# Performance work log

Hardware: AMD Instinct MI355X
Metric: run time of the kernel (lower is better)

## Reference

```python
import jax, jax.numpy as jnp
import numpy as np

B, L, E, H, D = 32, 512, 256, 8, 64
SCALE = int(D ** 0.5)  # matches TF: int(hidden_dim ** 0.5) == 8


def setup_inputs() -> dict:
    key = jax.random.key(0)
    ks = jax.random.split(key, 6)
    return {
        "x": jax.random.normal(ks[0], (B, L, E), dtype=jnp.float32),
        "positional": jax.random.normal(ks[1], (L, E), dtype=jnp.float32) * 0.02,
        "Wq": jax.random.normal(ks[2], (H, E, D), dtype=jnp.float32) * 0.05,
        "Wk": jax.random.normal(ks[3], (H, E, D), dtype=jnp.float32) * 0.05,
        "Wv": jax.random.normal(ks[4], (H, E, D), dtype=jnp.float32) * 0.05,
        "Wo": jax.random.normal(ks[5], (H * D, E), dtype=jnp.float32) * 0.05,
    }


def reference(x, positional, Wq, Wk, Wv, Wo):
    act = jnp.tanh  # activation='tanh'
    xp = x + positional                                   # [B,L,E]
    # Batched per-head projections with activation applied post-matmul
    q = act(jnp.einsum('ble,hed->bhld', xp, Wq))          # [B,H,L,D]
    k = act(jnp.einsum('ble,hed->bhld', xp, Wk))
    v = act(jnp.einsum('ble,hed->bhld', xp, Wv))
    score = jnp.einsum('bhqd,bhkd->bhqk', q, k) / SCALE   # [B,H,L,L]
    attn = jax.nn.softmax(score, axis=-1)
    out = jnp.einsum('bhqk,bhkd->bhqd', attn, v)          # [B,H,L,D]
    # concat heads along last axis (head-major) -> [B,L,H*D]
    out = jnp.transpose(out, (0, 2, 1, 3)).reshape(B, L, H * D)
    return jnp.einsum('blf,fe->ble', out, Wo) + act(xp)   # [B,L,E]
```

## Files before the change

### kernel.cpp

```cpp
#include <hip/hip_runtime.h>
#include <cstdint>

#define NB 32
#define NL 512
#define NE 256
#define NH 8
#define ND 64
#define NM 16384
#define NHD 512

using half8  = __attribute__((ext_vector_type(8))) _Float16;
using half4  = __attribute__((ext_vector_type(4))) _Float16;
using f32x4  = __attribute__((ext_vector_type(4))) float;
using f32x16 = __attribute__((ext_vector_type(16))) float;
using u32x2  = __attribute__((ext_vector_type(2))) unsigned int;

__device__ __forceinline__ f32x4 mfma16(half8 a, half8 b, f32x4 c) {
    return __builtin_amdgcn_mfma_f32_16x16x32_f16(a, b, c, 0, 0, 0);
}
__device__ __forceinline__ f32x16 mfma32(half8 a, half8 b, f32x16 c) {
    return __builtin_amdgcn_mfma_f32_32x32x16_f16(a, b, c, 0, 0, 0);
}
__device__ __forceinline__ void cp16_g2l(const void* g, void* l) {
    __builtin_amdgcn_global_load_lds(
        (const __attribute__((address_space(1))) void*)g,
        (__attribute__((address_space(3))) void*)l, 16, 0, 0);
}
__device__ __forceinline__ float exp2fast(float x) {
    return __builtin_amdgcn_exp2f(x);
}
__device__ __forceinline__ float fast_tanh(float x) {
    float xc = fminf(fmaxf(x, -9.f), 9.f);
    float t = exp2fast(xc * 2.88539008178f);
    return (t - 1.f) * __builtin_amdgcn_rcpf(t + 1.f);
}
__device__ __forceinline__ uint32_t pk16(float a, float b) {
    auto h2 = __builtin_amdgcn_cvt_pkrtz(a, b);
    return __builtin_bit_cast(uint32_t, h2);
}

__global__ __launch_bounds__(256) void prep(
        const float* __restrict__ x, const float* __restrict__ pos,
        const float* __restrict__ Wq, const float* __restrict__ Wk,
        const float* __restrict__ Wv, const float* __restrict__ Wo,
        _Float16* __restrict__ wqkv, _Float16* __restrict__ woh,
        _Float16* __restrict__ xph) {
    int bid = blockIdx.x;
    if (bid < 2048) {
        int idx = bid * 256 + threadIdx.x;
        if (idx < 1536 * 256) {
            int n = idx >> 8, e = idx & 255;
            int s = n >> 9, h = (n >> 6) & 7, d = n & 63;
            const float* W = (s == 0) ? Wq : (s == 1) ? Wk : Wv;
            wqkv[idx] = (_Float16)W[(h * NE + e) * ND + d];
        } else {
            int j = idx - 1536 * 256;
            int e = j >> 9, f = j & 511;
            woh[j] = (_Float16)Wo[f * NE + e];
        }
    } else {
        int i = ((bid - 2048) * 256 + threadIdx.x) * 4;
        float4 xv = *(const float4*)(x + i);
        float4 pv = *(const float4*)(pos + (i & (NL * NE - 1)));
        half4 o;
        o[0] = (_Float16)(xv.x + pv.x);
        o[1] = (_Float16)(xv.y + pv.y);
        o[2] = (_Float16)(xv.z + pv.z);
        o[3] = (_Float16)(xv.w + pv.w);
        *(half4*)(xph + i) = o;
    }
}

__global__ __launch_bounds__(256) void proj_gemm(
        const _Float16* __restrict__ wqkv, const _Float16* __restrict__ xph,
        _Float16* __restrict__ q_all, _Float16* __restrict__ k_all,
        _Float16* __restrict__ vT) {
    __shared__ _Float16 Alds[2][128 * 64];
    __shared__ _Float16 Blds[2][128 * 64];
    int tid = threadIdx.x;
    int w = tid >> 6, l = tid & 63;
    int bid = blockIdx.x;
    int xcd = bid & 7, local = bid >> 3;
    int tn = local % 12;
    int tm = xcd * 16 + local / 12;
    int wn = w >> 1, wm = w & 1;
    int m16 = l & 15, g = l >> 4;
    bool isv = (tn >= 8);
    int lrow8 = l >> 3;
    int kc16 = (l & 7) ^ lrow8;
    f32x4 acc[4][4] = {};

    const _Float16* Ag = wqkv + (size_t)tn * 128 * 256;
    const _Float16* Bg = xph + (size_t)tm * 128 * 256;

#define PROJ_STAGE(kt, buf)                                                   \
    _Pragma("unroll") for (int i = 0; i < 4; ++i) {                           \
        int cA = w * 4 + i;                                                   \
        int row = cA * 8 + lrow8;                                             \
        cp16_g2l(Ag + (size_t)row * 256 + (kt) * 64 + kc16 * 8,               \
                 &Alds[buf][cA * 512]);                                       \
        cp16_g2l(Bg + (size_t)row * 256 + (kt) * 64 + kc16 * 8,               \
                 &Blds[buf][cA * 512]);                                       \
    }

    PROJ_STAGE(0, 0);
    __syncthreads();
    int cur = 0;
    for (int kt = 0; kt < 4; ++kt) {
        if (kt < 3) { PROJ_STAGE(kt + 1, cur ^ 1); }
#pragma unroll
        for (int ks = 0; ks < 2; ++ks) {
            half8 af[4], bf[4];
#pragma unroll
            for (int f = 0; f < 4; ++f) {
                int ra = wn * 64 + f * 16 + m16;
                int rb = wm * 64 + f * 16 + m16;
                af[f] = *(const half8*)(&Alds[cur][ra * 64 + (((ks * 4 + g) ^ (ra & 7)) << 3)]);
                bf[f] = *(const half8*)(&Blds[cur][rb * 64 + (((ks * 4 + g) ^ (rb & 7)) << 3)]);
            }
            if (!isv) {
#pragma unroll
                for (int nf = 0; nf < 4; ++nf)
#pragma unroll
                    for (int mf = 0; mf < 4; ++mf)
                        acc[nf][mf] = mfma16(af[nf], bf[mf], acc[nf][mf]);
            } else {
#pragma unroll
                for (int nf = 0; nf < 4; ++nf)
#pragma unroll
                    for (int mf = 0; mf < 4; ++mf)
                        acc[nf][mf] = mfma16(bf[mf], af[nf], acc[nf][mf]);
            }
        }
        __syncthreads();
        cur ^= 1;
    }
#undef PROJ_STAGE
    if (!isv) {
        _Float16* dst = (tn < 4) ? q_all : k_all;
#pragma unroll
        for (int nf = 0; nf < 4; ++nf) {
            int c = (tn & 3) * 128 + wn * 64 + nf * 16 + g * 4;
#pragma unroll
            for (int mf = 0; mf < 4; ++mf) {
                int m = tm * 128 + wm * 64 + mf * 16 + m16;
                f32x4 v = acc[nf][mf];
                half4 hv;
#pragma unroll
                for (int r = 0; r < 4; ++r) hv[r] = (_Float16)fast_tanh(v[r]);
                *(half4*)(dst + (size_t)m * NHD + c) = hv;
            }
        }
    } else {
#pragma unroll
        for (int nf = 0; nf < 4; ++nf) {
            int c = (tn - 8) * 128 + wn * 64 + nf * 16 + m16;
#pragma unroll
            for (int mf = 0; mf < 4; ++mf) {
                int t0 = tm * 128 + wm * 64 + mf * 16 + g * 4;
                f32x4 v = acc[nf][mf];
                half4 hv;
#pragma unroll
                for (int r = 0; r < 4; ++r) hv[r] = (_Float16)fast_tanh(v[r]);
                *(half4*)(vT + (size_t)c * NM + t0) = hv;
            }
        }
    }
}

__global__ __launch_bounds__(256, 3) void attn_kernel(
        const _Float16* __restrict__ q_all, const _Float16* __restrict__ k_all,
        const _Float16* __restrict__ vT, _Float16* __restrict__ attn_out) {
    __shared__ _Float16 Klds[2][64 * 64];
    __shared__ _Float16 Vtlds[2][64 * 64];
    int tid = threadIdx.x;
    int w = tid >> 6, l = tid & 63;
    int l31 = l & 31, hi = l >> 5;
    int bid = blockIdx.x;
    int qt = bid & 3, h = (bid >> 2) & 7, b = bid >> 5;
    const float C1 = 0.125f * 1.44269504089f;

    int qbase = qt * 128 + w * 32;
    half8 qf[4];
    {
        const _Float16* qp = q_all + (size_t)(b * NL + qbase + l31) * NHD + h * ND + hi * 8;
#pragma unroll
        for (int ks = 0; ks < 4; ++ks) qf[ks] = *(const half8*)(qp + ks * 16);
    }

    f32x16 acc_o[2] = {};
    float mrow = -1e30f, lrow = 0.f;

    int st_row = tid >> 2;
    int st_u0 = (tid & 3) * 2;
    const _Float16* kg = k_all + (size_t)(b * NL + st_row) * NHD + h * ND + st_u0 * 8;
    const _Float16* vg = vT + (size_t)(h * ND + st_row) * NM + b * NL + st_u0 * 8;
    int so0 = st_row * 64 + ((st_u0 ^ (st_row & 7)) << 3);
    int so1 = st_row * 64 + (((st_u0 + 1) ^ (st_row & 7)) << 3);

    uint4 kv0 = *(const uint4*)(kg);
    uint4 kv1 = *(const uint4*)(kg + 8);
    uint4 vv0 = *(const uint4*)(vg);
    uint4 vv1 = *(const uint4*)(vg + 8);
    *(uint4*)&Klds[0][so0] = kv0;   *(uint4*)&Klds[0][so1] = kv1;
    *(uint4*)&Vtlds[0][so0] = vv0;  *(uint4*)&Vtlds[0][so1] = vv1;
    __syncthreads();

    for (int kt = 0; kt < 8; ++kt) {
        int cur = kt & 1;
        if (kt < 7) {
            const _Float16* kp = kg + (size_t)(kt + 1) * 64 * NHD;
            const _Float16* vp = vg + (kt + 1) * 64;
            kv0 = *(const uint4*)(kp);      kv1 = *(const uint4*)(kp + 8);
            vv0 = *(const uint4*)(vp);      vv1 = *(const uint4*)(vp + 8);
        }
        f32x16 acc_s[2] = {};
        __builtin_amdgcn_s_setprio(1);
#pragma unroll
        for (int ks = 0; ks < 4; ++ks)
#pragma unroll
            for (int kb2 = 0; kb2 < 2; ++kb2) {
                int key = kb2 * 32 + l31;
                half8 kb = *(const half8*)(&Klds[cur][key * 64 + (((ks * 2 + hi) ^ (key & 7)) << 3)]);
                acc_s[kb2] = mfma32(kb, qf[ks], acc_s[kb2]);
            }
        __builtin_amdgcn_s_setprio(0);
        float mx = -1e30f;
#pragma unroll
        for (int kb2 = 0; kb2 < 2; ++kb2)
#pragma unroll
            for (int j = 0; j < 16; ++j) mx = fmaxf(mx, acc_s[kb2][j]);
        mx = fmaxf(mx, __shfl_xor(mx, 32));
        mx *= 0.125f;
        if (!__all(mx <= mrow + 8.f)) {
            float mn = fmaxf(mrow, mx);
            float alpha = exp2fast((mrow - mn) * 1.44269504089f);
            mrow = mn;
            lrow *= alpha;
            float aq[16];
#pragma unroll
            for (int c = 0; c < 4; ++c)
#pragma unroll
                for (int r = 0; r < 4; ++r)
                    aq[c * 4 + r] = __shfl(alpha, c * 8 + hi * 4 + r);
#pragma unroll
            for (int d2 = 0; d2 < 2; ++d2)
#pragma unroll
                for (int j = 0; j < 16; ++j) acc_o[d2][j] *= aq[j];
        }
        float ml = mrow * 1.44269504089f;
        float rs = 0.f;
        uint32_t cw[2][4][2];
#pragma unroll
        for (int kb2 = 0; kb2 < 2; ++kb2)
#pragma unroll
            for (int a = 0; a < 4; ++a)
#pragma unroll
                for (int p = 0; p < 2; ++p) {
                    float p0 = exp2fast(fmaf(acc_s[kb2][4 * a + 2 * p],     C1, -ml));
                    float p1 = exp2fast(fmaf(acc_s[kb2][4 * a + 2 * p + 1], C1, -ml));
                    rs += p0 + p1;
                    cw[kb2][a][p] = pk16(p0, p1);
                }
        rs += __shfl_xor(rs, 32);
        lrow += rs;
        __builtin_amdgcn_s_setprio(1);
#pragma unroll
        for (int ks = 0; ks < 4; ++ks) {
            int kb2 = ks >> 1, s = ks & 1;
            u32x2 r0 = __builtin_amdgcn_permlane32_swap(
                cw[kb2][2 * s][0], cw[kb2][2 * s + 1][0], false, false);
            u32x2 r1 = __builtin_amdgcn_permlane32_swap(
                cw[kb2][2 * s][1], cw[kb2][2 * s + 1][1], false, false);
            union { uint32_t u[4]; half8 h; } pu;
            pu.u[0] = r0[0];  pu.u[1] = r1[0];
            pu.u[2] = r0[1];  pu.u[3] = r1[1];
#pragma unroll
            for (int d2 = 0; d2 < 2; ++d2) {
                int d = d2 * 32 + l31;
                half8 vb = *(const half8*)(&Vtlds[cur][d * 64 + (((ks * 2 + hi) ^ (d & 7)) << 3)]);
                acc_o[d2] = mfma32(pu.h, vb, acc_o[d2]);
            }
        }
        __builtin_amdgcn_s_setprio(0);
        if (kt < 7) {
            int nxt = cur ^ 1;
            *(uint4*)&Klds[nxt][so0] = kv0;   *(uint4*)&Klds[nxt][so1] = kv1;
            *(uint4*)&Vtlds[nxt][so0] = vv0;  *(uint4*)&Vtlds[nxt][so1] = vv1;
            __syncthreads();
        }
    }
    size_t orow0 = (size_t)(b * NL + qbase);
#pragma unroll
    for (int c = 0; c < 4; ++c)
#pragma unroll
        for (int r = 0; r < 4; ++r) {
            int qrow = c * 8 + hi * 4 + r;
            float inv = 1.f / __shfl(lrow, qrow);
#pragma unroll
            for (int d2 = 0; d2 < 2; ++d2)
                attn_out[(orow0 + qrow) * NHD + h * ND + d2 * 32 + l31] =
                    (_Float16)(acc_o[d2][c * 4 + r] * inv);
        }
}

__global__ __launch_bounds__(256) void final_gemm(
        const _Float16* __restrict__ woh, const _Float16* __restrict__ attn,
        const _Float16* __restrict__ xph, float* __restrict__ out) {
    __shared__ _Float16 Alds[2][128 * 64];
    __shared__ _Float16 Blds[2][64 * 64];
    int tid = threadIdx.x;
    int w = tid >> 6, l = tid & 63;
    int tn = blockIdx.x & 1, tm = blockIdx.x >> 1;
    int wn = w >> 1, wm = w & 1;
    int m16 = l & 15, g = l >> 4;
    int lrow8 = l >> 3;
    int kc16 = (l & 7) ^ lrow8;
    f32x4 acc[4][2] = {};

    const _Float16* Ag = woh + (size_t)tn * 128 * 512;
    const _Float16* Bg = attn + (size_t)tm * 64 * 512;

#define FIN_STAGE(kt, buf)                                                    \
    _Pragma("unroll") for (int i = 0; i < 4; ++i) {                           \
        int cA = w * 4 + i;                                                   \
        int row = cA * 8 + lrow8;                                             \
        cp16_g2l(Ag + (size_t)row * 512 + (kt) * 64 + kc16 * 8,               \
                 &Alds[buf][cA * 512]);                                       \
    }                                                                         \
    _Pragma("unroll") for (int i = 0; i < 2; ++i) {                           \
        int cB = w * 2 + i;                                                   \
        int row = cB * 8 + lrow8;                                             \
        cp16_g2l(Bg + (size_t)row * 512 + (kt) * 64 + kc16 * 8,               \
                 &Blds[buf][cB * 512]);                                       \
    }

    FIN_STAGE(0, 0);
    __syncthreads();
    int cur = 0;
    for (int kt = 0; kt < 8; ++kt) {
        if (kt < 7) { FIN_STAGE(kt + 1, cur ^ 1); }
#pragma unroll
        for (int ks = 0; ks < 2; ++ks) {
            half8 af[4], bf[2];
#pragma unroll
            for (int f = 0; f < 4; ++f) {
                int ra = wn * 64 + f * 16 + m16;
                af[f] = *(const half8*)(&Alds[cur][ra * 64 + (((ks * 4 + g) ^ (ra & 7)) << 3)]);
            }
#pragma unroll
            for (int f = 0; f < 2; ++f) {
                int rb = wm * 32 + f * 16 + m16;
                bf[f] = *(const half8*)(&Blds[cur][rb * 64 + (((ks * 4 + g) ^ (rb & 7)) << 3)]);
            }
#pragma unroll
            for (int nf = 0; nf < 4; ++nf)
#pragma unroll
                for (int mf = 0; mf < 2; ++mf)
                    acc[nf][mf] = mfma16(af[nf], bf[mf], acc[nf][mf]);
        }
        __syncthreads();
        cur ^= 1;
    }
#undef FIN_STAGE
#pragma unroll
    for (int nf = 0; nf < 4; ++nf) {
        int e = tn * 128 + wn * 64 + nf * 16 + g * 4;
#pragma unroll
        for (int mf = 0; mf < 2; ++mf) {
            int m = tm * 64 + wm * 32 + mf * 16 + m16;
            half4 hx = *(const half4*)(xph + (size_t)m * NE + e);
            f32x4 v = acc[nf][mf];
            float4 o;
            o.x = v[0] + fast_tanh((float)hx[0]);
            o.y = v[1] + fast_tanh((float)hx[1]);
            o.z = v[2] + fast_tanh((float)hx[2]);
            o.w = v[3] + fast_tanh((float)hx[3]);
            *(float4*)(out + (size_t)m * NE + e) = o;
        }
    }
}

extern "C" void kernel_launch(void* const* d_in, const int* in_sizes, int n_in,
                              void* d_out, int out_size, void* d_ws, size_t ws_size,
                              hipStream_t stream) {
    const float* x   = (const float*)d_in[0];
    const float* pos = (const float*)d_in[1];
    const float* Wq  = (const float*)d_in[2];
    const float* Wk  = (const float*)d_in[3];
    const float* Wv  = (const float*)d_in[4];
    const float* Wo  = (const float*)d_in[5];
    float* out = (float*)d_out;

    char* ws = (char*)d_ws;
    _Float16* xph   = (_Float16*)(ws);
    _Float16* wqkv  = (_Float16*)(ws + 8388608);
    _Float16* woh   = (_Float16*)(ws + 9175040);
    _Float16* q_all = (_Float16*)(ws + 9437184);
    _Float16* k_all = (_Float16*)(ws + 26214400);
    _Float16* vT    = (_Float16*)(ws + 42991616);
    _Float16* attn  = (_Float16*)(ws + 59768832);

    prep<<<dim3(6144), dim3(256), 0, stream>>>(x, pos, Wq, Wk, Wv, Wo, wqkv, woh, xph);
    proj_gemm<<<dim3(12 * 128), dim3(256), 0, stream>>>(wqkv, xph, q_all, k_all, vT);
    attn_kernel<<<dim3(1024), dim3(256), 0, stream>>>(q_all, k_all, vT, attn);
    final_gemm<<<dim3(512), dim3(256), 0, stream>>>(woh, attn, xph, out);
}
```

Before: 85.36 us.

## Fuse x+positional add into projection and final GEMMs, drop xph buffer

The prep kernel no longer builds an fp16 x+pos buffer. proj_gemm now loads fp32 x and pos through registers, adds them, converts to fp16 and writes the result into swizzled LDS. The LDS write is placed after the MFMA work so the global loads overlap compute. final_gemm reads fp32 x and pos directly for the tanh residual. The attention kernel's row max is also rewritten as a tree reduction. This removes one write and one read of an intermediate, but proj_gemm now reads twice as many bytes for B (fp32 x plus pos) across all 12 N-tiles, adds register pressure, and replaces the asynchronous global-to-LDS copy with a register round trip.

Result: slower. 100.3 us (+17.4%).

```diff
diff --git a/kernel.cpp b/kernel.cpp
--- a/kernel.cpp
+++ b/kernel.cpp
@@ -40,39 +40,25 @@
 }
 
 __global__ __launch_bounds__(256) void prep(
-        const float* __restrict__ x, const float* __restrict__ pos,
         const float* __restrict__ Wq, const float* __restrict__ Wk,
         const float* __restrict__ Wv, const float* __restrict__ Wo,
-        _Float16* __restrict__ wqkv, _Float16* __restrict__ woh,
-        _Float16* __restrict__ xph) {
-    int bid = blockIdx.x;
-    if (bid < 2048) {
-        int idx = bid * 256 + threadIdx.x;
-        if (idx < 1536 * 256) {
-            int n = idx >> 8, e = idx & 255;
-            int s = n >> 9, h = (n >> 6) & 7, d = n & 63;
-            const float* W = (s == 0) ? Wq : (s == 1) ? Wk : Wv;
-            wqkv[idx] = (_Float16)W[(h * NE + e) * ND + d];
-        } else {
-            int j = idx - 1536 * 256;
-            int e = j >> 9, f = j & 511;
-            woh[j] = (_Float16)Wo[f * NE + e];
-        }
+        _Float16* __restrict__ wqkv, _Float16* __restrict__ woh) {
+    int idx = blockIdx.x * 256 + threadIdx.x;
+    if (idx < 1536 * 256) {
+        int n = idx >> 8, e = idx & 255;
+        int s = n >> 9, h = (n >> 6) & 7, d = n & 63;
+        const float* W = (s == 0) ? Wq : (s == 1) ? Wk : Wv;
+        wqkv[idx] = (_Float16)W[(h * NE + e) * ND + d];
     } else {
-        int i = ((bid - 2048) * 256 + threadIdx.x) * 4;
-        float4 xv = *(const float4*)(x + i);
-        float4 pv = *(const float4*)(pos + (i & (NL * NE - 1)));
-        half4 o;
-        o[0] = (_Float16)(xv.x + pv.x);
-        o[1] = (_Float16)(xv.y + pv.y);
-        o[2] = (_Float16)(xv.z + pv.z);
-        o[3] = (_Float16)(xv.w + pv.w);
-        *(half4*)(xph + i) = o;
+        int j = idx - 1536 * 256;
+        int e = j >> 9, f = j & 511;
+        woh[j] = (_Float16)Wo[f * NE + e];
     }
 }
 
 __global__ __launch_bounds__(256) void proj_gemm(
-        const _Float16* __restrict__ wqkv, const _Float16* __restrict__ xph,
+        const _Float16* __restrict__ wqkv, const float* __restrict__ x,
+        const float* __restrict__ pos,
         _Float16* __restrict__ q_all, _Float16* __restrict__ k_all,
         _Float16* __restrict__ vT) {
     __shared__ _Float16 Alds[2][128 * 64];
@@ -88,26 +74,54 @@
     bool isv = (tn >= 8);
     int lrow8 = l >> 3;
     int kc16 = (l & 7) ^ lrow8;
+    int br = tid >> 2;
+    int bc = tid & 3;
     f32x4 acc[4][4] = {};
 
     const _Float16* Ag = wqkv + (size_t)tn * 128 * 256;
-    const _Float16* Bg = xph + (size_t)tm * 128 * 256;
-
-#define PROJ_STAGE(kt, buf)                                                   \
+    const float* Xg = x + (size_t)(tm * 128) * 256;
+    const float* Pg = pos + (size_t)((tm & 3) * 128) * 256;
+
+    float4 xr[2][4], pr[2][4];
+#define PROJ_LOADB(kt)                                                        \
+    _Pragma("unroll") for (int p = 0; p < 2; ++p) {                           \
+        int row = p * 64 + br;                                                \
+        const float* xp = Xg + (size_t)row * 256 + (kt) * 64 + bc * 16;       \
+        const float* pp = Pg + (size_t)row * 256 + (kt) * 64 + bc * 16;       \
+        _Pragma("unroll") for (int j = 0; j < 4; ++j) {                       \
+            xr[p][j] = *(const float4*)(xp + j * 4);                          \
+            pr[p][j] = *(const float4*)(pp + j * 4);                          \
+        }                                                                     \
+    }
+#define PROJ_WRITEB(buf)                                                      \
+    _Pragma("unroll") for (int p = 0; p < 2; ++p) {                           \
+        int row = p * 64 + br;                                                \
+        _Pragma("unroll") for (int c2 = 0; c2 < 2; ++c2) {                    \
+            half8 hv;                                                         \
+            _Pragma("unroll") for (int e = 0; e < 8; ++e) {                   \
+                const float* xf = (const float*)&xr[p][c2 * 2 + (e >> 2)];    \
+                const float* pf = (const float*)&pr[p][c2 * 2 + (e >> 2)];    \
+                hv[e] = (_Float16)(xf[e & 3] + pf[e & 3]);                    \
+            }                                                                 \
+            int unit = bc * 2 + c2;                                           \
+            *(half8*)(&Blds[buf][row * 64 + ((unit ^ (row & 7)) << 3)]) = hv; \
+        }                                                                     \
+    }
+#define PROJ_STAGE_A(kt, buf)                                                 \
     _Pragma("unroll") for (int i = 0; i < 4; ++i) {                           \
         int cA = w * 4 + i;                                                   \
         int row = cA * 8 + lrow8;                                             \
         cp16_g2l(Ag + (size_t)row * 256 + (kt) * 64 + kc16 * 8,               \
                  &Alds[buf][cA * 512]);                                       \
-        cp16_g2l(Bg + (size_t)row * 256 + (kt) * 64 + kc16 * 8,               \
-                 &Blds[buf][cA * 512]);                                       \
-    }
-
-    PROJ_STAGE(0, 0);
+    }
+
+    PROJ_LOADB(0);
+    PROJ_STAGE_A(0, 0);
+    PROJ_WRITEB(0);
     __syncthreads();
     int cur = 0;
     for (int kt = 0; kt < 4; ++kt) {
-        if (kt < 3) { PROJ_STAGE(kt + 1, cur ^ 1); }
+        if (kt < 3) { PROJ_LOADB(kt + 1); PROJ_STAGE_A(kt + 1, cur ^ 1); }
 #pragma unroll
         for (int ks = 0; ks < 2; ++ks) {
             half8 af[4], bf[4];
@@ -132,10 +146,13 @@
                         acc[nf][mf] = mfma16(bf[mf], af[nf], acc[nf][mf]);
             }
         }
+        if (kt < 3) { PROJ_WRITEB(cur ^ 1); }
         __syncthreads();
         cur ^= 1;
     }
-#undef PROJ_STAGE
+#undef PROJ_LOADB
+#undef PROJ_WRITEB
+#undef PROJ_STAGE_A
     if (!isv) {
         _Float16* dst = (tn < 4) ? q_all : k_all;
 #pragma unroll
@@ -229,7 +246,11 @@
 #pragma unroll
         for (int kb2 = 0; kb2 < 2; ++kb2)
 #pragma unroll
-            for (int j = 0; j < 16; ++j) mx = fmaxf(mx, acc_s[kb2][j]);
+            for (int j = 0; j < 16; j += 4) {
+                float a = fmaxf(fmaxf(acc_s[kb2][j], acc_s[kb2][j + 1]),
+                                acc_s[kb2][j + 2]);
+                mx = fmaxf(fmaxf(mx, a), acc_s[kb2][j + 3]);
+            }
         mx = fmaxf(mx, __shfl_xor(mx, 32));
         mx *= 0.125f;
         if (!__all(mx <= mrow + 8.f)) {
@@ -306,7 +327,8 @@
 
 __global__ __launch_bounds__(256) void final_gemm(
         const _Float16* __restrict__ woh, const _Float16* __restrict__ attn,
-        const _Float16* __restrict__ xph, float* __restrict__ out) {
+        const float* __restrict__ x, const float* __restrict__ pos,
+        float* __restrict__ out) {
     __shared__ _Float16 Alds[2][128 * 64];
     __shared__ _Float16 Blds[2][64 * 64];
     int tid = threadIdx.x;
@@ -369,13 +391,15 @@
 #pragma unroll
         for (int mf = 0; mf < 2; ++mf) {
             int m = tm * 64 + wm * 32 + mf * 16 + m16;
-            half4 hx = *(const half4*)(xph + (size_t)m * NE + e);
+            int lr = m & (NL - 1);
+            float4 xv = *(const float4*)(x + (size_t)m * NE + e);
+            float4 pv = *(const float4*)(pos + (size_t)lr * NE + e);
             f32x4 v = acc[nf][mf];
             float4 o;
-            o.x = v[0] + fast_tanh((float)hx[0]);
-            o.y = v[1] + fast_tanh((float)hx[1]);
-            o.z = v[2] + fast_tanh((float)hx[2]);
-            o.w = v[3] + fast_tanh((float)hx[3]);
+            o.x = v[0] + fast_tanh(xv.x + pv.x);
+            o.y = v[1] + fast_tanh(xv.y + pv.y);
+            o.z = v[2] + fast_tanh(xv.z + pv.z);
+            o.w = v[3] + fast_tanh(xv.w + pv.w);
             *(float4*)(out + (size_t)m * NE + e) = o;
         }
     }
@@ -393,16 +417,15 @@
     float* out = (float*)d_out;
 
     char* ws = (char*)d_ws;
-    _Float16* xph   = (_Float16*)(ws);
-    _Float16* wqkv  = (_Float16*)(ws + 8388608);
-    _Float16* woh   = (_Float16*)(ws + 9175040);
-    _Float16* q_all = (_Float16*)(ws + 9437184);
-    _Float16* k_all = (_Float16*)(ws + 26214400);
-    _Float16* vT    = (_Float16*)(ws + 42991616);
-    _Float16* attn  = (_Float16*)(ws + 59768832);
-
-    prep<<<dim3(6144), dim3(256), 0, stream>>>(x, pos, Wq, Wk, Wv, Wo, wqkv, woh, xph);
-    proj_gemm<<<dim3(12 * 128), dim3(256), 0, stream>>>(wqkv, xph, q_all, k_all, vT);
+    _Float16* wqkv  = (_Float16*)(ws);
+    _Float16* woh   = (_Float16*)(ws + 786432);
+    _Float16* q_all = (_Float16*)(ws + 1048576);
+    _Float16* k_all = (_Float16*)(ws + 17825792);
+    _Float16* vT    = (_Float16*)(ws + 34603008);
+    _Float16* attn  = (_Float16*)(ws + 51380224);
+
+    prep<<<dim3(2048), dim3(256), 0, stream>>>(Wq, Wk, Wv, Wo, wqkv, woh);
+    proj_gemm<<<dim3(12 * 128), dim3(256), 0, stream>>>(wqkv, x, pos, q_all, k_all, vT);
     attn_kernel<<<dim3(1024), dim3(256), 0, stream>>>(q_all, k_all, vT, attn);
-    final_gemm<<<dim3(512), dim3(256), 0, stream>>>(woh, attn, xph, out);
-}
+    final_gemm<<<dim3(512), dim3(256), 0, stream>>>(woh, attn, x, pos, out);
+}
```
